# Performance work log

Measured on AMD Instinct MI355X. Metric: run time of the kernel, lower is better.

The kernel has to match this reference:

```python
import jax, jax.numpy as jnp
import numpy as np

N_NODES = 50000
N_EDGES = 800000
IN_FEATS = 128
OUT_FEATS = 128


def setup_inputs() -> dict:
    key = jax.random.key(0)
    k_feat, k_src, k_dst, k_w1, k_w2, k_lw = jax.random.split(key, 6)
    feat = jax.random.normal(k_feat, (N_NODES, IN_FEATS), dtype=jnp.float32)
    src_idx = jax.random.randint(k_src, (N_EDGES,), 0, N_NODES, dtype=jnp.int64 if jax.config.jax_enable_x64 else jnp.int32)
    dst_idx = jax.random.randint(k_dst, (N_EDGES,), 0, N_NODES, dtype=jnp.int64 if jax.config.jax_enable_x64 else jnp.int32)
    # xavier-uniform-ish scales
    w1_lim = float(np.sqrt(6.0 / (2 * IN_FEATS + IN_FEATS)))
    w2_lim = float(np.sqrt(6.0 / (IN_FEATS + OUT_FEATS)))
    lw_lim = float(np.sqrt(2.0) * np.sqrt(6.0 / (IN_FEATS + OUT_FEATS)))
    weight1 = jax.random.uniform(k_w1, (2 * IN_FEATS, IN_FEATS), jnp.float32, -w1_lim, w1_lim)
    weight2 = jax.random.uniform(k_w2, (IN_FEATS, OUT_FEATS), jnp.float32, -w2_lim, w2_lim)
    loop_weight = jax.random.uniform(k_lw, (IN_FEATS, OUT_FEATS), jnp.float32, -lw_lim, lw_lim)
    bias = jnp.zeros((OUT_FEATS,), dtype=jnp.float32)
    return {
        "feat": feat,
        "src_idx": src_idx,
        "dst_idx": dst_idx,
        "weight1": weight1,
        "weight2": weight2,
        "loop_weight": loop_weight,
        "bias": bias,
    }


def reference(feat, src_idx, dst_idx, weight1, weight2, loop_weight, bias):
    # Gather per-edge src/dst features and concat: [E, 2*d]
    feat_msg = jnp.concatenate([feat[src_idx], feat[dst_idx]], axis=-1)
    # 2-layer edge MLP: relu(msg @ W1) @ W2 -> [E, out]
    e_msg = jnp.matmul(jax.nn.relu(jnp.matmul(feat_msg, weight1)), weight2)
    # Scatter-sum to destination nodes: [N, out]
    rst = jax.ops.segment_sum(e_msg, dst_idx, num_segments=feat.shape[0])
    # bias + residual loop message
    rst = rst + bias + jnp.matmul(feat, loop_weight)
    return rst
```

## Files before the change

### kernel.cpp

```cpp
#include <hip/hip_runtime.h>

typedef __attribute__((ext_vector_type(8))) unsigned short ushort8v;
typedef __attribute__((ext_vector_type(8))) short short8v;
typedef __attribute__((ext_vector_type(4))) float f32x4;

__device__ inline unsigned short f2bf(float f) {
    union { float f; unsigned u; } v; v.f = f;
    unsigned u = v.u;
    unsigned r = (u + 0x7FFFu + ((u >> 16) & 1u)) >> 16;
    return (unsigned short)r;
}
__device__ inline float bf2f(unsigned short h) {
    union { unsigned u; float f; } v; v.u = ((unsigned)h) << 16;
    return v.f;
}

#define CAP 64

__global__ __launch_bounds__(256) void fused_pre(
    const float* __restrict__ feat, unsigned short* __restrict__ X2, int totalF,
    const float* __restrict__ W1, const float* __restrict__ W2,
    const float* __restrict__ LW,
    unsigned short* __restrict__ W1t, unsigned short* __restrict__ W3t,
    int cvtB) {
    int b = blockIdx.x, t = threadIdx.x;
    if (b < cvtB) {
        int idx = (b * 256 + t) * 4;
        if (idx >= totalF) return;
        float4 v = *(const float4*)(feat + idx);
        int row = idx >> 7, col = idx & 127;
        unsigned short* o = X2 + (size_t)row * 256 + 128 + col;
        *(ushort4*)o = make_ushort4(f2bf(v.x), f2bf(v.y), f2bf(v.z), f2bf(v.w));
    } else {
        int i = (b - cvtB) * 256 + t;
        if (i < 32768) {
            int jj = i >> 7, k = i & 127;
            float v = (jj < 128) ? W1[k * 128 + jj] : W1[(128 + k) * 128 + (jj - 128)];
            W1t[i] = f2bf(v);
        } else {
            int i2 = i - 32768;
            int n = i2 >> 8, k = i2 & 255;
            float v = (k < 128) ? W2[k * 128 + n] : LW[(k - 128) * 128 + n];
            W3t[i2] = f2bf(v);
        }
    }
}

template <bool OUT_BF16>
__device__ void gemm_tile(
    unsigned short* As, unsigned short* Bs,
    const unsigned short* __restrict__ A, int lda,
    const unsigned short* __restrict__ Bt, int ldb, int nRowsB,
    void* __restrict__ Cout, int ldc,
    const float* __restrict__ bias, int M, int K, int m0, int n0) {
    const int tid = threadIdx.x;
    const int lane = tid & 63;
    const int w = tid >> 6;
    const int wr = w >> 1, wc = w & 1;
    const int q = lane >> 4, ln = lane & 15;

    f32x4 acc[4][4];
#pragma unroll
    for (int i = 0; i < 4; i++)
#pragma unroll
        for (int j = 0; j < 4; j++) acc[i][j] = (f32x4)0.f;

    for (int kk = 0; kk < K; kk += 64) {
#pragma unroll
        for (int i = 0; i < 4; i++) {
            int id = i * 256 + tid;
            int r = id >> 3, b = id & 7;
            ushort8v v = (ushort8v)(unsigned short)0;
            int gr = m0 + r;
            if (gr < M) v = *(const ushort8v*)(A + (size_t)gr * lda + kk + b * 8);
            *(ushort8v*)(As + r * 64 + ((b ^ (r & 7)) * 8)) = v;
        }
#pragma unroll
        for (int i = 0; i < 4; i++) {
            int id = i * 256 + tid;
            int r = id >> 3, b = id & 7;
            ushort8v v = (ushort8v)(unsigned short)0;
            int gr = n0 + r;
            if (gr < nRowsB) v = *(const ushort8v*)(Bt + (size_t)gr * ldb + kk + b * 8);
            *(ushort8v*)(Bs + r * 64 + ((b ^ (r & 7)) * 8)) = v;
        }
        __syncthreads();
#pragma unroll
        for (int ks = 0; ks < 2; ks++) {
            short8v af[4], bfv[4];
#pragma unroll
            for (int ti = 0; ti < 4; ti++) {
                int m = wr * 64 + ti * 16 + ln;
                int blk = (ks * 4 + q) ^ (m & 7);
                af[ti] = *(const short8v*)(As + m * 64 + blk * 8);
            }
#pragma unroll
            for (int tj = 0; tj < 4; tj++) {
                int n = wc * 64 + tj * 16 + ln;
                int blk = (ks * 4 + q) ^ (n & 7);
                bfv[tj] = *(const short8v*)(Bs + n * 64 + blk * 8);
            }
#pragma unroll
            for (int ti = 0; ti < 4; ti++)
#pragma unroll
                for (int tj = 0; tj < 4; tj++)
                    acc[ti][tj] = __builtin_amdgcn_mfma_f32_16x16x32_bf16(
                        af[ti], bfv[tj], acc[ti][tj], 0, 0, 0);
        }
        __syncthreads();
    }

#pragma unroll
    for (int ti = 0; ti < 4; ti++) {
        int rowb = m0 + wr * 64 + ti * 16 + q * 4;
#pragma unroll
        for (int tj = 0; tj < 4; tj++) {
            int col = n0 + wc * 64 + tj * 16 + ln;
            f32x4 c = acc[ti][tj];
            float bv = 0.f;
            if (!OUT_BF16 && bias) bv = bias[col];
#pragma unroll
            for (int r = 0; r < 4; r++) {
                int row = rowb + r;
                if (row < M) {
                    if (OUT_BF16)
                        ((unsigned short*)Cout)[(size_t)row * ldc + col] = f2bf(c[r]);
                    else
                        ((float*)Cout)[(size_t)row * ldc + col] = c[r] + bv;
                }
            }
        }
    }
}

__global__ __launch_bounds__(256) void gemm1_scatter(
    const unsigned short* __restrict__ X2feat, const unsigned short* __restrict__ W1t,
    unsigned short* __restrict__ AB,
    const int* __restrict__ src, const int* __restrict__ dst,
    int* __restrict__ cur, unsigned short* __restrict__ eSrc,
    int E, int gemmB, int N) {
    __shared__ unsigned short smem[2 * 128 * 64];
    int b = blockIdx.x;
    int half = b >> 1;
    if ((b & 1) == 0) {
        if (half >= gemmB) return;
        int m0 = (half >> 1) * 128, n0 = (half & 1) * 128;
        gemm_tile<true>(smem, smem + 128 * 64, X2feat, 256, W1t, 128, 256,
                        (void*)AB, 256, nullptr, N, 128, m0, n0);
    } else {
        int e = (half * 256 + threadIdx.x) * 4;
        if (e + 3 < E) {
            int4 s4 = *(const int4*)(src + e);
            int4 d4 = *(const int4*)(dst + e);
            int p0 = atomicAdd(&cur[d4.x], 1);
            int p1 = atomicAdd(&cur[d4.y], 1);
            int p2 = atomicAdd(&cur[d4.z], 1);
            int p3 = atomicAdd(&cur[d4.w], 1);
            eSrc[(size_t)d4.x * CAP + min(p0, CAP - 1)] = (unsigned short)s4.x;
            eSrc[(size_t)d4.y * CAP + min(p1, CAP - 1)] = (unsigned short)s4.y;
            eSrc[(size_t)d4.z * CAP + min(p2, CAP - 1)] = (unsigned short)s4.z;
            eSrc[(size_t)d4.w * CAP + min(p3, CAP - 1)] = (unsigned short)s4.w;
        } else {
            for (int i = e; i < E && i >= 0; i++) {
                int d = dst[i];
                int pos = atomicAdd(&cur[d], 1);
                eSrc[(size_t)d * CAP + min(pos, CAP - 1)] = (unsigned short)src[i];
            }
        }
    }
}

__global__ __launch_bounds__(256) void gather_kernel(
    const unsigned short* __restrict__ AB, const int* __restrict__ cur,
    const unsigned short* __restrict__ eSrc,
    unsigned short* __restrict__ X2, int N) {
    int wid = (blockIdx.x * 256 + threadIdx.x) >> 6;
    int lane = threadIdx.x & 63;
    if (wid >= N) return;
    int num = min(cur[wid], CAP);
    size_t start = (size_t)wid * CAP;
    int half = lane >> 5, ln32 = lane & 31;
    ushort4 bv = *(const ushort4*)(AB + (size_t)wid * 256 + 128 + ln32 * 4);
    float b0 = bf2f(bv.x), b1 = bf2f(bv.y), b2 = bf2f(bv.z), b3 = bf2f(bv.w);
    float p0 = 0.f, p1 = 0.f, p2 = 0.f, p3 = 0.f;

    int mySrc = (lane < num) ? (int)eSrc[start + lane] : 0;
    int j = 0;
    for (; j + 8 <= num; j += 8) {
        ushort4 v[4];
#pragma unroll
        for (int u = 0; u < 4; u++) {
            int s = __shfl(mySrc, j + 2 * u + half);
            v[u] = *(const ushort4*)(AB + (size_t)s * 256 + ln32 * 4);
        }
#pragma unroll
        for (int u = 0; u < 4; u++) {
            p0 += fmaxf(bf2f(v[u].x) + b0, 0.f);
            p1 += fmaxf(bf2f(v[u].y) + b1, 0.f);
            p2 += fmaxf(bf2f(v[u].z) + b2, 0.f);
            p3 += fmaxf(bf2f(v[u].w) + b3, 0.f);
        }
    }
    for (; j < num; j += 2) {
        int idx = j + half;
        int s = __shfl(mySrc, idx);
        bool ok = idx < num;
        ushort4 v = *(const ushort4*)(AB + (size_t)s * 256 + ln32 * 4);
        float m = ok ? 1.f : 0.f;
        p0 += m * fmaxf(bf2f(v.x) + b0, 0.f);
        p1 += m * fmaxf(bf2f(v.y) + b1, 0.f);
        p2 += m * fmaxf(bf2f(v.z) + b2, 0.f);
        p3 += m * fmaxf(bf2f(v.w) + b3, 0.f);
    }
    p0 += __shfl_xor(p0, 32);
    p1 += __shfl_xor(p1, 32);
    p2 += __shfl_xor(p2, 32);
    p3 += __shfl_xor(p3, 32);
    if (half == 0) {
        *(ushort4*)(X2 + (size_t)wid * 256 + ln32 * 4) =
            make_ushort4(f2bf(p0), f2bf(p1), f2bf(p2), f2bf(p3));
    }
}

template <bool OUT_BF16>
__global__ __launch_bounds__(256) void gemm128(
    const unsigned short* __restrict__ A, int lda,
    const unsigned short* __restrict__ Bt, int ldb, int nRowsB,
    void* __restrict__ Cout, int ldc,
    const float* __restrict__ bias, int M, int K) {
    __shared__ unsigned short smem[2 * 128 * 64];
    gemm_tile<OUT_BF16>(smem, smem + 128 * 64, A, lda, Bt, ldb, nRowsB,
                        Cout, ldc, bias, M, K, blockIdx.x * 128, blockIdx.y * 128);
}

extern "C" void kernel_launch(void* const* d_in, const int* in_sizes, int n_in,
                              void* d_out, int out_size, void* d_ws, size_t ws_size,
                              hipStream_t stream) {
    const float* feat = (const float*)d_in[0];
    const int* src = (const int*)d_in[1];
    const int* dst = (const int*)d_in[2];
    const float* W1 = (const float*)d_in[3];
    const float* W2 = (const float*)d_in[4];
    const float* LW = (const float*)d_in[5];
    const float* bias = (const float*)d_in[6];
    float* out = (float*)d_out;

    const int N = in_sizes[0] / 128;
    const int E = in_sizes[1];

    char* ws = (char*)d_ws;
    unsigned short* X2 = (unsigned short*)ws;
    size_t off_b = (size_t)N * 256 * 2;
    unsigned short* AB = (unsigned short*)(ws + off_b);
    off_b += (size_t)N * 256 * 2;
    unsigned short* W1t = (unsigned short*)(ws + off_b);
    off_b += (size_t)256 * 128 * 2;
    unsigned short* W3t = (unsigned short*)(ws + off_b);
    off_b += (size_t)128 * 256 * 2;
    int* cur = (int*)(ws + off_b);             off_b += (size_t)N * 4;
    unsigned short* eSrc = (unsigned short*)(ws + off_b);
    off_b += (size_t)N * CAP * 2;

    int totalF = N * 128;
    int cvtB = (totalF / 4 + 255) / 256;

    hipMemsetAsync(cur, 0, (size_t)N * 4, stream);
    fused_pre<<<cvtB + 256, 256, 0, stream>>>(
        feat, X2, totalF, W1, W2, LW, W1t, W3t, cvtB);

    int gemmB = ((N + 127) / 128) * 2;
    int scatB = ((E + 3) / 4 + 255) / 256;
    int mx = gemmB > scatB ? gemmB : scatB;
    gemm1_scatter<<<2 * mx, 256, 0, stream>>>(
        X2 + 128, W1t, AB, src, dst, cur, eSrc, E, gemmB, N);

    gather_kernel<<<(N + 3) / 4, 256, 0, stream>>>(AB, cur, eSrc, X2, N);

    dim3 g2((N + 127) / 128, 1);
    gemm128<false><<<g2, 256, 0, stream>>>(X2, 256, W3t, 256, 128,
                                           (void*)out, 128, bias, N, 256);
}
```

Measured before the change: 183.0 us.

## Fuse feat bf16 conversion into GEMM A-loads, pad atomic counters, deepen gather unroll

Drops the separate pass that converts the fp32 node features into a bf16 workspace. Both GEMMs now read fp32 feat directly and pack it to bf16 with v_cvt_pk_bf16_f32 while filling LDS, and the second GEMM takes its first half of K from a compact aggregate buffer. The per-node atomic counters are padded to a 32-int stride to spread contention, at the cost of a larger memset. The gather loop is unrolled to 16 edges with a 4-edge remainder step to keep more loads in flight.

```diff
diff --git a/kernel.cpp b/kernel.cpp
--- a/kernel.cpp
+++ b/kernel.cpp
@@ -3,6 +3,9 @@
 typedef __attribute__((ext_vector_type(8))) unsigned short ushort8v;
 typedef __attribute__((ext_vector_type(8))) short short8v;
 typedef __attribute__((ext_vector_type(4))) float f32x4;
+
+#define CAP 64
+#define CSTRIDE 32
 
 __device__ inline unsigned short f2bf(float f) {
     union { float f; unsigned u; } v; v.f = f;
@@ -14,42 +17,34 @@
     union { unsigned u; float f; } v; v.u = ((unsigned)h) << 16;
     return v.f;
 }
-
-#define CAP 64
-
-__global__ __launch_bounds__(256) void fused_pre(
-    const float* __restrict__ feat, unsigned short* __restrict__ X2, int totalF,
+__device__ inline unsigned pkbf(float lo, float hi) {
+    unsigned r;
+    asm("v_cvt_pk_bf16_f32 %0, %1, %2" : "=v"(r) : "v"(lo), "v"(hi));
+    return r;
+}
+
+__global__ __launch_bounds__(256) void prep_weights(
     const float* __restrict__ W1, const float* __restrict__ W2,
     const float* __restrict__ LW,
-    unsigned short* __restrict__ W1t, unsigned short* __restrict__ W3t,
-    int cvtB) {
-    int b = blockIdx.x, t = threadIdx.x;
-    if (b < cvtB) {
-        int idx = (b * 256 + t) * 4;
-        if (idx >= totalF) return;
-        float4 v = *(const float4*)(feat + idx);
-        int row = idx >> 7, col = idx & 127;
-        unsigned short* o = X2 + (size_t)row * 256 + 128 + col;
-        *(ushort4*)o = make_ushort4(f2bf(v.x), f2bf(v.y), f2bf(v.z), f2bf(v.w));
+    unsigned short* __restrict__ W1t, unsigned short* __restrict__ W3t) {
+    int i = blockIdx.x * 256 + threadIdx.x;
+    if (i < 32768) {
+        int jj = i >> 7, k = i & 127;
+        float v = (jj < 128) ? W1[k * 128 + jj] : W1[(128 + k) * 128 + (jj - 128)];
+        W1t[i] = f2bf(v);
     } else {
-        int i = (b - cvtB) * 256 + t;
-        if (i < 32768) {
-            int jj = i >> 7, k = i & 127;
-            float v = (jj < 128) ? W1[k * 128 + jj] : W1[(128 + k) * 128 + (jj - 128)];
-            W1t[i] = f2bf(v);
-        } else {
-            int i2 = i - 32768;
-            int n = i2 >> 8, k = i2 & 255;
-            float v = (k < 128) ? W2[k * 128 + n] : LW[(k - 128) * 128 + n];
-            W3t[i2] = f2bf(v);
-        }
-    }
-}
-
-template <bool OUT_BF16>
+        int i2 = i - 32768;
+        int n = i2 >> 8, k = i2 & 255;
+        float v = (k < 128) ? W2[k * 128 + n] : LW[(k - 128) * 128 + n];
+        W3t[i2] = f2bf(v);
+    }
+}
+
+template <int AMODE, bool OUT_BF16>
 __device__ void gemm_tile(
     unsigned short* As, unsigned short* Bs,
-    const unsigned short* __restrict__ A, int lda,
+    const unsigned short* __restrict__ Abf, int lda,
+    const float* __restrict__ Af32,
     const unsigned short* __restrict__ Bt, int ldb, int nRowsB,
     void* __restrict__ Cout, int ldc,
     const float* __restrict__ bias, int M, int K, int m0, int n0) {
@@ -66,23 +61,37 @@
         for (int j = 0; j < 4; j++) acc[i][j] = (f32x4)0.f;
 
     for (int kk = 0; kk < K; kk += 64) {
+        const bool aF32 = (AMODE == 1) || (AMODE == 2 && kk >= 128);
 #pragma unroll
         for (int i = 0; i < 4; i++) {
             int id = i * 256 + tid;
-            int r = id >> 3, b = id & 7;
-            ushort8v v = (ushort8v)(unsigned short)0;
+            int r = id >> 3, bb = id & 7;
             int gr = m0 + r;
-            if (gr < M) v = *(const ushort8v*)(A + (size_t)gr * lda + kk + b * 8);
-            *(ushort8v*)(As + r * 64 + ((b ^ (r & 7)) * 8)) = v;
+            unsigned short* dstp = As + r * 64 + ((bb ^ (r & 7)) * 8);
+            if (aF32) {
+                float4 lo = make_float4(0.f, 0.f, 0.f, 0.f), hi = lo;
+                if (gr < M) {
+                    const float* p = Af32 + (size_t)gr * 128 +
+                                     (AMODE == 2 ? kk - 128 : kk) + bb * 8;
+                    lo = *(const float4*)p;
+                    hi = *(const float4*)(p + 4);
+                }
+                *(uint4*)dstp = make_uint4(pkbf(lo.x, lo.y), pkbf(lo.z, lo.w),
+                                           pkbf(hi.x, hi.y), pkbf(hi.z, hi.w));
+            } else {
+                ushort8v v = (ushort8v)(unsigned short)0;
+                if (gr < M) v = *(const ushort8v*)(Abf + (size_t)gr * lda + kk + bb * 8);
+                *(ushort8v*)dstp = v;
+            }
         }
 #pragma unroll
         for (int i = 0; i < 4; i++) {
             int id = i * 256 + tid;
-            int r = id >> 3, b = id & 7;
+            int r = id >> 3, bb = id & 7;
             ushort8v v = (ushort8v)(unsigned short)0;
             int gr = n0 + r;
-            if (gr < nRowsB) v = *(const ushort8v*)(Bt + (size_t)gr * ldb + kk + b * 8);
-            *(ushort8v*)(Bs + r * 64 + ((b ^ (r & 7)) * 8)) = v;
+            if (gr < nRowsB) v = *(const ushort8v*)(Bt + (size_t)gr * ldb + kk + bb * 8);
+            *(ushort8v*)(Bs + r * 64 + ((bb ^ (r & 7)) * 8)) = v;
         }
         __syncthreads();
 #pragma unroll
@@ -134,7 +143,7 @@
 }
 
 __global__ __launch_bounds__(256) void gemm1_scatter(
-    const unsigned short* __restrict__ X2feat, const unsigned short* __restrict__ W1t,
+    const float* __restrict__ feat, const unsigned short* __restrict__ W1t,
     unsigned short* __restrict__ AB,
     const int* __restrict__ src, const int* __restrict__ dst,
     int* __restrict__ cur, unsigned short* __restrict__ eSrc,
@@ -145,17 +154,17 @@
     if ((b & 1) == 0) {
         if (half >= gemmB) return;
         int m0 = (half >> 1) * 128, n0 = (half & 1) * 128;
-        gemm_tile<true>(smem, smem + 128 * 64, X2feat, 256, W1t, 128, 256,
-                        (void*)AB, 256, nullptr, N, 128, m0, n0);
+        gemm_tile<1, true>(smem, smem + 128 * 64, nullptr, 0, feat, W1t, 128, 256,
+                           (void*)AB, 256, nullptr, N, 128, m0, n0);
     } else {
         int e = (half * 256 + threadIdx.x) * 4;
         if (e + 3 < E) {
             int4 s4 = *(const int4*)(src + e);
             int4 d4 = *(const int4*)(dst + e);
-            int p0 = atomicAdd(&cur[d4.x], 1);
-            int p1 = atomicAdd(&cur[d4.y], 1);
-            int p2 = atomicAdd(&cur[d4.z], 1);
-            int p3 = atomicAdd(&cur[d4.w], 1);
+            int p0 = atomicAdd(&cur[d4.x * CSTRIDE], 1);
+            int p1 = atomicAdd(&cur[d4.y * CSTRIDE], 1);
+            int p2 = atomicAdd(&cur[d4.z * CSTRIDE], 1);
+            int p3 = atomicAdd(&cur[d4.w * CSTRIDE], 1);
             eSrc[(size_t)d4.x * CAP + min(p0, CAP - 1)] = (unsigned short)s4.x;
             eSrc[(size_t)d4.y * CAP + min(p1, CAP - 1)] = (unsigned short)s4.y;
             eSrc[(size_t)d4.z * CAP + min(p2, CAP - 1)] = (unsigned short)s4.z;
@@ -163,7 +172,7 @@
         } else {
             for (int i = e; i < E && i >= 0; i++) {
                 int d = dst[i];
-                int pos = atomicAdd(&cur[d], 1);
+                int pos = atomicAdd(&cur[d * CSTRIDE], 1);
                 eSrc[(size_t)d * CAP + min(pos, CAP - 1)] = (unsigned short)src[i];
             }
         }
@@ -173,11 +182,11 @@
 __global__ __launch_bounds__(256) void gather_kernel(
     const unsigned short* __restrict__ AB, const int* __restrict__ cur,
     const unsigned short* __restrict__ eSrc,
-    unsigned short* __restrict__ X2, int N) {
+    unsigned short* __restrict__ S2, int N) {
     int wid = (blockIdx.x * 256 + threadIdx.x) >> 6;
     int lane = threadIdx.x & 63;
     if (wid >= N) return;
-    int num = min(cur[wid], CAP);
+    int num = min(cur[wid * CSTRIDE], CAP);
     size_t start = (size_t)wid * CAP;
     int half = lane >> 5, ln32 = lane & 31;
     ushort4 bv = *(const ushort4*)(AB + (size_t)wid * 256 + 128 + ln32 * 4);
@@ -186,15 +195,30 @@
 
     int mySrc = (lane < num) ? (int)eSrc[start + lane] : 0;
     int j = 0;
-    for (; j + 8 <= num; j += 8) {
-        ushort4 v[4];
-#pragma unroll
-        for (int u = 0; u < 4; u++) {
+    for (; j + 16 <= num; j += 16) {
+        ushort4 v[8];
+#pragma unroll
+        for (int u = 0; u < 8; u++) {
             int s = __shfl(mySrc, j + 2 * u + half);
             v[u] = *(const ushort4*)(AB + (size_t)s * 256 + ln32 * 4);
         }
 #pragma unroll
-        for (int u = 0; u < 4; u++) {
+        for (int u = 0; u < 8; u++) {
+            p0 += fmaxf(bf2f(v[u].x) + b0, 0.f);
+            p1 += fmaxf(bf2f(v[u].y) + b1, 0.f);
+            p2 += fmaxf(bf2f(v[u].z) + b2, 0.f);
+            p3 += fmaxf(bf2f(v[u].w) + b3, 0.f);
+        }
+    }
+    for (; j + 4 <= num; j += 4) {
+        ushort4 v[2];
+#pragma unroll
+        for (int u = 0; u < 2; u++) {
+            int s = __shfl(mySrc, j + 2 * u + half);
+            v[u] = *(const ushort4*)(AB + (size_t)s * 256 + ln32 * 4);
+        }
+#pragma unroll
+        for (int u = 0; u < 2; u++) {
             p0 += fmaxf(bf2f(v[u].x) + b0, 0.f);
             p1 += fmaxf(bf2f(v[u].y) + b1, 0.f);
             p2 += fmaxf(bf2f(v[u].z) + b2, 0.f);
@@ -217,20 +241,18 @@
     p2 += __shfl_xor(p2, 32);
     p3 += __shfl_xor(p3, 32);
     if (half == 0) {
-        *(ushort4*)(X2 + (size_t)wid * 256 + ln32 * 4) =
+        *(ushort4*)(S2 + (size_t)wid * 128 + ln32 * 4) =
             make_ushort4(f2bf(p0), f2bf(p1), f2bf(p2), f2bf(p3));
     }
 }
 
-template <bool OUT_BF16>
-__global__ __launch_bounds__(256) void gemm128(
-    const unsigned short* __restrict__ A, int lda,
-    const unsigned short* __restrict__ Bt, int ldb, int nRowsB,
-    void* __restrict__ Cout, int ldc,
-    const float* __restrict__ bias, int M, int K) {
+__global__ __launch_bounds__(256) void gemm2_kernel(
+    const unsigned short* __restrict__ S2, const float* __restrict__ feat,
+    const unsigned short* __restrict__ W3t,
+    float* __restrict__ out, const float* __restrict__ bias, int M) {
     __shared__ unsigned short smem[2 * 128 * 64];
-    gemm_tile<OUT_BF16>(smem, smem + 128 * 64, A, lda, Bt, ldb, nRowsB,
-                        Cout, ldc, bias, M, K, blockIdx.x * 128, blockIdx.y * 128);
+    gemm_tile<2, false>(smem, smem + 128 * 64, S2, 128, feat, W3t, 256, 128,
+                        (void*)out, 128, bias, M, 256, blockIdx.x * 128, 0);
 }
 
 extern "C" void kernel_launch(void* const* d_in, const int* in_sizes, int n_in,
@@ -249,34 +271,29 @@
     const int E = in_sizes[1];
 
     char* ws = (char*)d_ws;
-    unsigned short* X2 = (unsigned short*)ws;
-    size_t off_b = (size_t)N * 256 * 2;
-    unsigned short* AB = (unsigned short*)(ws + off_b);
-    off_b += (size_t)N * 256 * 2;
-    unsigned short* W1t = (unsigned short*)(ws + off_b);
-    off_b += (size_t)256 * 128 * 2;
-    unsigned short* W3t = (unsigned short*)(ws + off_b);
-    off_b += (size_t)128 * 256 * 2;
-    int* cur = (int*)(ws + off_b);             off_b += (size_t)N * 4;
-    unsigned short* eSrc = (unsigned short*)(ws + off_b);
-    off_b += (size_t)N * CAP * 2;
-
-    int totalF = N * 128;
-    int cvtB = (totalF / 4 + 255) / 256;
-
-    hipMemsetAsync(cur, 0, (size_t)N * 4, stream);
-    fused_pre<<<cvtB + 256, 256, 0, stream>>>(
-        feat, X2, totalF, W1, W2, LW, W1t, W3t, cvtB);
+    unsigned short* S2 = (unsigned short*)ws;
+    size_t off = (size_t)N * 128 * 2;
+    unsigned short* AB = (unsigned short*)(ws + off);
+    off += (size_t)N * 256 * 2;
+    unsigned short* W1t = (unsigned short*)(ws + off);
+    off += (size_t)256 * 128 * 2;
+    unsigned short* W3t = (unsigned short*)(ws + off);
+    off += (size_t)128 * 256 * 2;
+    int* cur = (int*)(ws + off);
+    off += (size_t)N * CSTRIDE * 4;
+    unsigned short* eSrc = (unsigned short*)(ws + off);
+    off += (size_t)N * CAP * 2;
+
+    hipMemsetAsync(cur, 0, (size_t)N * CSTRIDE * 4, stream);
+    prep_weights<<<256, 256, 0, stream>>>(W1, W2, LW, W1t, W3t);
 
     int gemmB = ((N + 127) / 128) * 2;
     int scatB = ((E + 3) / 4 + 255) / 256;
     int mx = gemmB > scatB ? gemmB : scatB;
     gemm1_scatter<<<2 * mx, 256, 0, stream>>>(
-        X2 + 128, W1t, AB, src, dst, cur, eSrc, E, gemmB, N);
-
-    gather_kernel<<<(N + 3) / 4, 256, 0, stream>>>(AB, cur, eSrc, X2, N);
-
-    dim3 g2((N + 127) / 128, 1);
-    gemm128<false><<<g2, 256, 0, stream>>>(X2, 256, W3t, 256, 128,
-                                           (void*)out, 128, bias, N, 256);
-}
+        feat, W1t, AB, src, dst, cur, eSrc, E, gemmB, N);
+
+    gather_kernel<<<(N + 3) / 4, 256, 0, stream>>>(AB, cur, eSrc, S2, N);
+
+    gemm2_kernel<<<(N + 127) / 128, 256, 0, stream>>>(S2, feat, W3t, out, bias, N);
+}
```

After: 181.6 us. About the same (-0.8%).
